# Kernel optimization log

Hardware: AMD Instinct MI355X
Metric: run time of the kernel (lower is better)

Reference implementation:

```python
import jax, jax.numpy as jnp
import numpy as np

TOKENS = 8192
DIM = 4096
N_EXPERTS = 256
TOPK = 8
N_GROUPS = 8
TOPK_GROUPS = 4
ROUTE_SCALE = 2.5


def setup_inputs() -> dict:
    key = jax.random.key(0)
    k1, k2, k3 = jax.random.split(key, 3)
    x = jax.random.normal(k1, (TOKENS, DIM), dtype=jnp.float32)
    W = jax.random.normal(k2, (N_EXPERTS, DIM), dtype=jnp.float32) * (DIM ** -0.5)
    bias = jax.random.normal(k3, (N_EXPERTS,), dtype=jnp.float32) * 0.01
    return {"x": x, "W": W, "bias": bias}


def reference(x, W, bias):
    T = x.shape[0]
    # linear scoring: [T, E]
    logits = jnp.einsum("td,ed->te", x, W)
    scores = jax.nn.sigmoid(logits)  # score_func == 'sigmoid'
    original_scores = scores
    s = scores + bias  # bias-corrected scores used only for routing
    # group-limited routing: [T, G, E/G]
    sg = s.reshape(T, N_GROUPS, -1)
    # bias is not None -> group score = sum of top-2 within each group
    group_scores = jax.lax.top_k(sg, 2)[0].sum(axis=-1)  # [T, G]
    gidx = jax.lax.top_k(group_scores, TOPK_GROUPS)[1]  # [T, topk_groups]
    mask = jnp.zeros((T, N_GROUPS), dtype=s.dtype).at[
        jnp.arange(T)[:, None], gidx
    ].set(1.0)
    s_masked = (sg * mask[:, :, None]).reshape(T, -1)  # [T, E]
    # final top-k over masked scores
    indices = jax.lax.top_k(s_masked, TOPK)[1]  # [T, topk] int32
    weights = jnp.take_along_axis(original_scores, indices, axis=1)
    # sigmoid path: renormalize selected weights
    weights = weights / weights.sum(axis=-1, keepdims=True)
    weights = weights * ROUTE_SCALE
    return weights.astype(x.dtype), indices
```

## Files before the change

kernel.cpp:

```cpp
#include <hip/hip_runtime.h>
#include <math.h>

#define TOKENS 8192
#define DIM 4096
#define NEXP 256
#define TK 8
#define ROUTE_SCALE 2.5f
#define TH1 1e-5f
#define TH2 2e-5f

#define PITCH 40

typedef _Float16 half8 __attribute__((ext_vector_type(8)));
typedef float f4 __attribute__((ext_vector_type(4)));
union H8 { half8 v; int4 q; };

__global__ __launch_bounds__(256) void wsplit(const float* __restrict__ W,
                                              _Float16* __restrict__ Whp,
                                              _Float16* __restrict__ Wlp,
                                              int* __restrict__ flag_cnt) {
    int fi = blockIdx.x * 256 + threadIdx.x;
    if (fi == 0) *flag_cnt = 0;
    int lane = fi & 63;
    int kc = (fi >> 6) & 127;
    int et = fi >> 13;
    int e = et * 16 + (lane & 15);
    int k = kc * 32 + ((lane >> 4) << 3);
    const float* src = W + (size_t)e * DIM + k;
    float4 a = *(const float4*)src;
    float4 b = *(const float4*)(src + 4);
    float f[8] = {a.x, a.y, a.z, a.w, b.x, b.y, b.z, b.w};
    H8 hh, hl;
#pragma unroll
    for (int j = 0; j < 8; j++) {
        float ws = f[j] * 256.0f;
        _Float16 h = (_Float16)ws;
        float r = ws - (float)h;
        hh.v[j] = h;
        hl.v[j] = (_Float16)(r * 2048.0f);
    }
    *(int4*)(Whp + (size_t)fi * 8) = hh.q;
    *(int4*)(Wlp + (size_t)fi * 8) = hl.q;
}

__global__ __launch_bounds__(256, 3) void score_gemm(const float* __restrict__ x,
                                                     const _Float16* __restrict__ Whp,
                                                     const _Float16* __restrict__ Wlp,
                                                     float* __restrict__ parts) {
    __shared__ __align__(16) _Float16 sAh[2][64 * PITCH];
    __shared__ __align__(16) _Float16 sAl[2][64 * PITCH];

    const int m0 = blockIdx.x * 64;
    const int nb = blockIdx.y;
    const int chunk = blockIdx.z;
    const int kcb = 43 * chunk;
    const int kce = kcb + (chunk == 2 ? 42 : 43);

    const int tid = threadIdx.x;
    const int lane = tid & 63;
    const int wave = tid >> 6;
    const int et0 = nb * 8 + wave * 2;

    const int srow = tid >> 2;
    const int scol = (tid & 3) * 8;
    const int sidx = srow * PITCH + scol;
    const float* xrow = x + (size_t)(m0 + srow) * DIM + scol;

    f4 accH[4][2], accC[4][2];
#pragma unroll
    for (int i = 0; i < 4; i++)
#pragma unroll
        for (int j = 0; j < 2; j++) { accH[i][j] = (f4)0.0f; accC[i][j] = (f4)0.0f; }

    float4 ra[2][2];
    half8 bh[2][2], bl[2][2];

#define LOADRAW(S, KC)                                                         \
    {                                                                          \
        const float* p_ = xrow + (size_t)(KC) * 32;                            \
        ra[S][0] = *(const float4*)p_;                                         \
        ra[S][1] = *(const float4*)(p_ + 4);                                   \
    }

#define CONV(S, B_)                                                            \
    {                                                                          \
        float f_[8] = {ra[S][0].x, ra[S][0].y, ra[S][0].z, ra[S][0].w,         \
                       ra[S][1].x, ra[S][1].y, ra[S][1].z, ra[S][1].w};        \
        H8 hh_, hl_;                                                           \
        _Pragma("unroll") for (int j_ = 0; j_ < 8; j_++) {                     \
            float xv_ = f_[j_] * 16.0f;                                        \
            _Float16 hv_ = (_Float16)xv_;                                      \
            float r_ = xv_ - (float)hv_;                                       \
            hh_.v[j_] = hv_;                                                   \
            hl_.v[j_] = (_Float16)(r_ * 2048.0f);                              \
        }                                                                      \
        *(int4*)&sAh[B_][sidx] = hh_.q;                                        \
        *(int4*)&sAl[B_][sidx] = hl_.q;                                        \
    }

#define BLOAD(P_, KC)                                                          \
    _Pragma("unroll") for (int nt_ = 0; nt_ < 2; nt_++) {                      \
        size_t o_ = ((size_t)((et0 + nt_) * 128 + (KC)) * 64 + lane) * 8;      \
        bh[P_][nt_] = *(const half8*)(Whp + o_);                               \
        bl[P_][nt_] = *(const half8*)(Wlp + o_);                               \
    }

#define MFMA_PHASE(P)                                                          \
    _Pragma("unroll") for (int mt_ = 0; mt_ < 4; mt_++) {                      \
        int ra_ = (mt_ * 16 + (lane & 15)) * PITCH + ((lane >> 4) << 3);       \
        half8 ah_ = *(const half8*)&sAh[P][ra_];                               \
        half8 al_ = *(const half8*)&sAl[P][ra_];                               \
        _Pragma("unroll") for (int nt_ = 0; nt_ < 2; nt_++) {                  \
            accH[mt_][nt_] = __builtin_amdgcn_mfma_f32_16x16x32_f16(           \
                ah_, bh[P][nt_], accH[mt_][nt_], 0, 0, 0);                     \
            accC[mt_][nt_] = __builtin_amdgcn_mfma_f32_16x16x32_f16(           \
                ah_, bl[P][nt_], accC[mt_][nt_], 0, 0, 0);                     \
            accC[mt_][nt_] = __builtin_amdgcn_mfma_f32_16x16x32_f16(           \
                al_, bh[P][nt_], accC[mt_][nt_], 0, 0, 0);                     \
        }                                                                      \
    }

#define BARRIER() asm volatile("s_waitcnt lgkmcnt(0)\n\ts_barrier" ::: "memory")

#define ITER(KC, P)                                                            \
    {                                                                          \
        if ((KC) + 1 < kce) { BLOAD(P ^ 1, (KC) + 1) }                         \
        if ((KC) + 2 < kce) { LOADRAW(P, (KC) + 2) }                           \
        MFMA_PHASE(P)                                                          \
        if ((KC) + 1 < kce) { CONV(P ^ 1, P ^ 1) }                             \
        BARRIER();                                                             \
    }

    LOADRAW(0, kcb)
    CONV(0, 0)
    LOADRAW(1, kcb + 1)
    BLOAD(0, kcb)
    BARRIER();

    int kc = kcb;
    while (kc + 2 <= kce) {
        ITER(kc, 0)
        ITER(kc + 1, 1)
        kc += 2;
    }
    if (kc < kce) { ITER(kc, 0) }

    float* pc = parts + (size_t)chunk * TOKENS * NEXP;
#pragma unroll
    for (int mt = 0; mt < 4; mt++)
#pragma unroll
        for (int nt = 0; nt < 2; nt++) {
            int m = m0 + mt * 16 + ((lane >> 4) << 2);
            int e = (et0 + nt) * 16 + (lane & 15);
#pragma unroll
            for (int r = 0; r < 4; r++)
                pc[(size_t)(m + r) * NEXP + e] =
                    accH[mt][nt][r] + accC[mt][nt][r] * (1.0f / 2048.0f);
        }
#undef LOADRAW
#undef CONV
#undef BLOAD
#undef MFMA_PHASE
#undef BARRIER
#undef ITER
}

__global__ __launch_bounds__(256) void route_kernel(const float* __restrict__ parts,
                                                    const float* __restrict__ bias,
                                                    float* __restrict__ out_w,
                                                    float* __restrict__ out_i,
                                                    int* __restrict__ flag_cnt,
                                                    int* __restrict__ flag_list) {
    const int t = blockIdx.x * 4 + (threadIdx.x >> 6);
    const int l = threadIdx.x & 63;

    const float* p = parts + (size_t)t * NEXP + (l << 2);
    float4 q0 = *(const float4*)p;
    float4 q1 = *(const float4*)(p + (size_t)TOKENS * NEXP);
    float4 q2 = *(const float4*)(p + (size_t)2 * TOKENS * NEXP);
    float4 b4 = *(const float4*)&bias[l << 2];
    float sc[4], sb[4];
    {
        float lg0 = (q0.x + q1.x + q2.x) * (1.0f / 4096.0f);
        float lg1 = (q0.y + q1.y + q2.y) * (1.0f / 4096.0f);
        float lg2 = (q0.z + q1.z + q2.z) * (1.0f / 4096.0f);
        float lg3 = (q0.w + q1.w + q2.w) * (1.0f / 4096.0f);
        sc[0] = 1.0f / (1.0f + expf(-lg0));
        sc[1] = 1.0f / (1.0f + expf(-lg1));
        sc[2] = 1.0f / (1.0f + expf(-lg2));
        sc[3] = 1.0f / (1.0f + expf(-lg3));
        sb[0] = sc[0] + b4.x; sb[1] = sc[1] + b4.y;
        sb[2] = sc[2] + b4.z; sb[3] = sc[3] + b4.w;
    }

    float v1 = sb[0], v2 = -1e30f, v3 = -1e30f;
#pragma unroll
    for (int c = 1; c < 4; c++) {
        float xv = sb[c];
        if (xv > v1) { v3 = v2; v2 = v1; v1 = xv; }
        else if (xv > v2) { v3 = v2; v2 = xv; }
        else if (xv > v3) { v3 = xv; }
    }

#pragma unroll
    for (int m = 1; m < 8; m <<= 1) {
        float o1 = __shfl_xor(v1, m, 64);
        float o2 = __shfl_xor(v2, m, 64);
        float o3 = __shfl_xor(v3, m, 64);
        bool aw = (v1 >= o1);
        float A1 = aw ? v1 : o1, A2 = aw ? v2 : o2, A3 = aw ? v3 : o3;
        float B1 = aw ? o1 : v1, B2 = aw ? o2 : v2;
        float n2, n3;
        if (A2 >= B1) { n2 = A2; n3 = fmaxf(B1, A3); }
        else          { n2 = B1; n3 = fmaxf(A2, B2); }
        v1 = A1; v2 = n2; v3 = n3;
    }
    float gscore = v1 + v2;
    float gap23 = v2 - v3;
#pragma unroll
    for (int m = 8; m < 64; m <<= 1) gap23 = fminf(gap23, __shfl_xor(gap23, m, 64));

    float gs[8];
#pragma unroll
    for (int g = 0; g < 8; g++) gs[g] = __shfl(gscore, g << 3, 64);

    const int mygrp = l >> 3;
    int rank = 0;
#pragma unroll
    for (int g = 0; g < 8; g++) {
        bool better = (gs[g] > gscore) || (gs[g] == gscore && g < mygrp);
        rank += (g != mygrp && better) ? 1 : 0;
    }
    const bool sel = rank < 4;

    float minsel = 1e30f, maxuns = -1e30f;
#pragma unroll
    for (int g = 0; g < 8; g++) {
        int rg = 0;
#pragma unroll
        for (int g2 = 0; g2 < 8; g2++)
            rg += (g2 != g && ((gs[g2] > gs[g]) || (gs[g2] == gs[g] && g2 < g))) ? 1 : 0;
        if (rg < 4) minsel = fminf(minsel, gs[g]); else maxuns = fmaxf(maxuns, gs[g]);
    }
    float gap45 = minsel - maxuns;

    float cand[4];
#pragma unroll
    for (int c = 0; c < 4; c++) cand[c] = sel ? sb[c] : 0.0f;

    float wv[8], wi[8], vb[9];
    float wsum = 0.0f;
#pragma unroll
    for (int r = 0; r < 9; r++) {
        float v = cand[0];
        int idx = (l << 2);
#pragma unroll
        for (int c = 1; c < 4; c++) {
            if (cand[c] > v) { v = cand[c]; idx = (l << 2) + c; }
        }
#pragma unroll
        for (int m = 32; m >= 1; m >>= 1) {
            float ov = __shfl_xor(v, m, 64);
            int oi = __shfl_xor(idx, m, 64);
            if (ov > v || (ov == v && oi < idx)) { v = ov; idx = oi; }
        }
        vb[r] = v;
        if (r < 8) {
            const int cc = idx & 3;
            const bool own = (idx >> 2) == l;
            cand[0] = (own && cc == 0) ? -__builtin_inff() : cand[0];
            cand[1] = (own && cc == 1) ? -__builtin_inff() : cand[1];
            cand[2] = (own && cc == 2) ? -__builtin_inff() : cand[2];
            cand[3] = (own && cc == 3) ? -__builtin_inff() : cand[3];
            float tmp = (cc == 0) ? sc[0] : (cc == 1) ? sc[1] : (cc == 2) ? sc[2] : sc[3];
            float ws = __shfl(tmp, idx >> 2, 64);
            wv[r] = ws;
            wi[r] = (float)idx;
            wsum += ws;
        }
    }
    float mingap = 1e30f;
#pragma unroll
    for (int r = 0; r < 8; r++) mingap = fminf(mingap, vb[r] - vb[r + 1]);

    const float scale = ROUTE_SCALE / wsum;
    if (l == 0) {
        float* ow = out_w + (size_t)t * TK;
        float* oi = out_i + (size_t)t * TK;
#pragma unroll
        for (int r = 0; r < 8; r++) ow[r] = wv[r] * scale;
#pragma unroll
        for (int r = 0; r < 8; r++) oi[r] = wi[r];
        if (gap23 < TH1 || gap45 < TH2 || mingap < TH1) {
            int pos = atomicAdd(flag_cnt, 1);
            flag_list[pos] = t;
        }
    }
}

__global__ __launch_bounds__(256) void fixup_kernel(const float* __restrict__ x,
                                                    const float* __restrict__ W,
                                                    const float* __restrict__ bias,
                                                    const int* __restrict__ flag_cnt,
                                                    const int* __restrict__ flag_list,
                                                    float* __restrict__ out_w,
                                                    float* __restrict__ out_i) {
    __shared__ float S[NEXP];
    const int n = *flag_cnt;
    for (int i = blockIdx.x; i < n; i += gridDim.x) {
        const int t = flag_list[i];
        const float* xr = x + (size_t)t * DIM;
        const float* wr = W + (size_t)threadIdx.x * DIM;
        float acc = 0.0f;
        for (int k = 0; k < DIM; k += 4) {
            float4 xv = *(const float4*)(xr + k);
            float4 wv = *(const float4*)(wr + k);
            acc = fmaf(xv.x, wv.x, acc);
            acc = fmaf(xv.y, wv.y, acc);
            acc = fmaf(xv.z, wv.z, acc);
            acc = fmaf(xv.w, wv.w, acc);
        }
        S[threadIdx.x] = 1.0f / (1.0f + expf(-acc));
        __syncthreads();
        if (threadIdx.x < 64) {
            const int l = threadIdx.x;
            float sc[4] = {S[4 * l], S[4 * l + 1], S[4 * l + 2], S[4 * l + 3]};
            float4 b4 = *(const float4*)&bias[4 * l];
            float sb[4] = {sc[0] + b4.x, sc[1] + b4.y, sc[2] + b4.z, sc[3] + b4.w};

            float h1 = fmaxf(sb[0], sb[1]), q1 = fminf(sb[0], sb[1]);
            float h2 = fmaxf(sb[2], sb[3]), q2 = fminf(sb[2], sb[3]);
            float m1 = fmaxf(h1, h2);
            float m2 = fmaxf(fminf(h1, h2), fmaxf(q1, q2));
#pragma unroll
            for (int m = 1; m < 8; m <<= 1) {
                float o1 = __shfl_xor(m1, m, 64);
                float o2 = __shfl_xor(m2, m, 64);
                float nm1 = fmaxf(m1, o1);
                float nm2 = fmaxf(fminf(m1, o1), fmaxf(m2, o2));
                m1 = nm1; m2 = nm2;
            }
            float gscore = m1 + m2;
            float gs[8];
#pragma unroll
            for (int g = 0; g < 8; g++) gs[g] = __shfl(gscore, g << 3, 64);
            const int mygrp = l >> 3;
            int rank = 0;
#pragma unroll
            for (int g = 0; g < 8; g++) {
                bool better = (gs[g] > gscore) || (gs[g] == gscore && g < mygrp);
                rank += (g != mygrp && better) ? 1 : 0;
            }
            const bool selg = rank < 4;
            float cand[4];
#pragma unroll
            for (int c = 0; c < 4; c++) cand[c] = selg ? sb[c] : 0.0f;
            float wv[8], wi[8];
            float wsum = 0.0f;
#pragma unroll
            for (int r = 0; r < 8; r++) {
                float v = cand[0];
                int idx = (l << 2);
#pragma unroll
                for (int c = 1; c < 4; c++) {
                    if (cand[c] > v) { v = cand[c]; idx = (l << 2) + c; }
                }
#pragma unroll
                for (int m = 32; m >= 1; m >>= 1) {
                    float ov = __shfl_xor(v, m, 64);
                    int oi = __shfl_xor(idx, m, 64);
                    if (ov > v || (ov == v && oi < idx)) { v = ov; idx = oi; }
                }
                const int cc = idx & 3;
                const bool own = (idx >> 2) == l;
                cand[0] = (own && cc == 0) ? -__builtin_inff() : cand[0];
                cand[1] = (own && cc == 1) ? -__builtin_inff() : cand[1];
                cand[2] = (own && cc == 2) ? -__builtin_inff() : cand[2];
                cand[3] = (own && cc == 3) ? -__builtin_inff() : cand[3];
                float tmp = (cc == 0) ? sc[0] : (cc == 1) ? sc[1] : (cc == 2) ? sc[2] : sc[3];
                float ws = __shfl(tmp, idx >> 2, 64);
                wv[r] = ws;
                wi[r] = (float)idx;
                wsum += ws;
            }
            const float scale = ROUTE_SCALE / wsum;
            if (l == 0) {
                float* ow = out_w + (size_t)t * TK;
                float* oi = out_i + (size_t)t * TK;
#pragma unroll
                for (int r = 0; r < 8; r++) ow[r] = wv[r] * scale;
#pragma unroll
                for (int r = 0; r < 8; r++) oi[r] = wi[r];
            }
        }
        __syncthreads();
    }
}

extern "C" void kernel_launch(void* const* d_in, const int* in_sizes, int n_in,
                              void* d_out, int out_size, void* d_ws, size_t ws_size,
                              hipStream_t stream) {
    const float* x = (const float*)d_in[0];
    const float* W = (const float*)d_in[1];
    const float* bias = (const float*)d_in[2];
    float* out = (float*)d_out;

    char* ws = (char*)d_ws;
    float* parts = (float*)ws;
    _Float16* Whp = (_Float16*)(ws + (size_t)3 * TOKENS * NEXP * 4);
    _Float16* Wlp = Whp + (size_t)NEXP * DIM;
    int* flag_cnt = (int*)((char*)(Wlp + (size_t)NEXP * DIM));
    int* flag_list = flag_cnt + 4;

    wsplit<<<512, 256, 0, stream>>>(W, Whp, Wlp, flag_cnt);

    dim3 gGemm(TOKENS / 64, 2, 3);
    score_gemm<<<gGemm, 256, 0, stream>>>(x, Whp, Wlp, parts);

    route_kernel<<<TOKENS / 4, 256, 0, stream>>>(parts, bias, out,
                                                 out + (size_t)TOKENS * TK,
                                                 flag_cnt, flag_list);
    fixup_kernel<<<1024, 256, 0, stream>>>(x, W, bias, flag_cnt, flag_list,
                                           out, out + (size_t)TOKENS * TK);
}
```

Measured before the change: 363.4 us.

## Stage x in LDS and software-pipeline W row loads in fixup kernel

The fixup kernel now copies each flagged token's x row into shared memory and keeps a large register buffer of W values, prefetching the next chunk while computing the current one. The grid shrinks from 1024 to 256 blocks with launch bounds allowing one block per CU. This targets the latency of serially streaming a 16KB W row per thread. The cost is very high register use, with a risk of spills, and less parallelism across flagged tokens.

```diff
diff --git a/kernel.cpp b/kernel.cpp
--- a/kernel.cpp
+++ b/kernel.cpp
@@ -298,27 +298,54 @@
     }
 }
 
-__global__ __launch_bounds__(256) void fixup_kernel(const float* __restrict__ x,
-                                                    const float* __restrict__ W,
-                                                    const float* __restrict__ bias,
-                                                    const int* __restrict__ flag_cnt,
-                                                    const int* __restrict__ flag_list,
-                                                    float* __restrict__ out_w,
-                                                    float* __restrict__ out_i) {
+__global__ __launch_bounds__(256, 1) void fixup_kernel(const float* __restrict__ x,
+                                                       const float* __restrict__ W,
+                                                       const float* __restrict__ bias,
+                                                       const int* __restrict__ flag_cnt,
+                                                       const int* __restrict__ flag_list,
+                                                       float* __restrict__ out_w,
+                                                       float* __restrict__ out_i) {
     __shared__ float S[NEXP];
+    __shared__ __align__(16) float sx[DIM];
     const int n = *flag_cnt;
     for (int i = blockIdx.x; i < n; i += gridDim.x) {
         const int t = flag_list[i];
         const float* xr = x + (size_t)t * DIM;
+#pragma unroll
+        for (int j = 0; j < 4; j++) {
+            const int idx = (j * 256 + threadIdx.x) * 4;
+            *(float4*)&sx[idx] = *(const float4*)(xr + idx);
+        }
+        __syncthreads();
+
         const float* wr = W + (size_t)threadIdx.x * DIM;
+        float4 wb[8][8];
+#pragma unroll
+        for (int d = 0; d < 8; d++)
+#pragma unroll
+            for (int q = 0; q < 8; q++)
+                wb[d][q] = *(const float4*)(wr + d * 32 + q * 4);
+
         float acc = 0.0f;
-        for (int k = 0; k < DIM; k += 4) {
-            float4 xv = *(const float4*)(xr + k);
-            float4 wv = *(const float4*)(wr + k);
-            acc = fmaf(xv.x, wv.x, acc);
-            acc = fmaf(xv.y, wv.y, acc);
-            acc = fmaf(xv.z, wv.z, acc);
-            acc = fmaf(xv.w, wv.w, acc);
+        for (int s16 = 0; s16 < 16; s16++) {
+#pragma unroll
+            for (int d = 0; d < 8; d++) {
+                const int s = s16 * 8 + d;
+#pragma unroll
+                for (int q = 0; q < 8; q++) {
+                    const float4 wv = wb[d][q];
+                    const float4 xv = *(const float4*)&sx[s * 32 + q * 4];
+                    acc = fmaf(xv.x, wv.x, acc);
+                    acc = fmaf(xv.y, wv.y, acc);
+                    acc = fmaf(xv.z, wv.z, acc);
+                    acc = fmaf(xv.w, wv.w, acc);
+                }
+                if (s16 < 15) {
+#pragma unroll
+                    for (int q = 0; q < 8; q++)
+                        wb[d][q] = *(const float4*)(wr + (s + 8) * 32 + q * 4);
+                }
+            }
         }
         S[threadIdx.x] = 1.0f / (1.0f + expf(-acc));
         __syncthreads();
@@ -420,6 +447,6 @@
     route_kernel<<<TOKENS / 4, 256, 0, stream>>>(parts, bias, out,
                                                  out + (size_t)TOKENS * TK,
                                                  flag_cnt, flag_list);
-    fixup_kernel<<<1024, 256, 0, stream>>>(x, W, bias, flag_cnt, flag_list,
-                                           out, out + (size_t)TOKENS * TK);
+    fixup_kernel<<<256, 256, 0, stream>>>(x, W, bias, flag_cnt, flag_list,
+                                          out, out + (size_t)TOKENS * TK);
 }
```

Result: slower. 371.9 us (+2.3%).

## Pipeline fixup kernel W loads through LDS with async global-to-LDS ring buffer

Applied to the files above, without the earlier changes.

Rewrites the exact fp32 fixup kernel so that the token row is staged once in shared memory and W columns stream through a 4-deep LDS ring using global_load_lds with XOR swizzling. The old version had each thread read its own strided W row and the x row straight from global memory. The new version aims to coalesce loads and overlap the memory traffic with the FMAs. It also cuts the grid from 1024 to 256 blocks with launch_bounds(256,1), which trades occupancy for explicit pipelining and risks lower throughput when many tokens are flagged.

```diff
diff --git a/kernel.cpp b/kernel.cpp
--- a/kernel.cpp
+++ b/kernel.cpp
@@ -298,32 +298,87 @@
     }
 }
 
-__global__ __launch_bounds__(256) void fixup_kernel(const float* __restrict__ x,
-                                                    const float* __restrict__ W,
-                                                    const float* __restrict__ bias,
-                                                    const int* __restrict__ flag_cnt,
-                                                    const int* __restrict__ flag_list,
-                                                    float* __restrict__ out_w,
-                                                    float* __restrict__ out_i) {
+__device__ __forceinline__ void gload16(const float* g, float* l) {
+    __builtin_amdgcn_global_load_lds(
+        (const __attribute__((address_space(1))) void*)g,
+        (__attribute__((address_space(3))) void*)l, 16, 0, 0);
+}
+
+__global__ __launch_bounds__(256, 1) void fixup_kernel(const float* __restrict__ x,
+                                                       const float* __restrict__ W,
+                                                       const float* __restrict__ bias,
+                                                       const int* __restrict__ flag_cnt,
+                                                       const int* __restrict__ flag_list,
+                                                       float* __restrict__ out_w,
+                                                       float* __restrict__ out_i) {
     __shared__ float S[NEXP];
+    __shared__ __align__(16) float sx[DIM];
+    __shared__ __align__(16) float ring[4][NEXP * 32];
+
+    const int tid = threadIdx.x;
+    const int lane = tid & 63;
+    const int wave = tid >> 6;
+
+#define STAGE(P, C)                                                            \
+    {                                                                          \
+        const int e_ = wave * 64 + (lane >> 3);                                \
+        const int q_ = (lane & 7) ^ ((lane >> 3) & 7);                         \
+        _Pragma("unroll") for (int j_ = 0; j_ < 8; j_++) {                     \
+            gload16(W + (size_t)(e_ + j_ * 8) * DIM + (C) * 32 + q_ * 4,       \
+                    &ring[P][(wave * 8 + j_) * 256]);                          \
+        }                                                                      \
+    }
+
+#define COMPUTE(P, C)                                                          \
+    {                                                                          \
+        const float* xb_ = sx + (C) * 32;                                      \
+        _Pragma("unroll") for (int q_ = 0; q_ < 8; q_++) {                     \
+            const int qq_ = q_ ^ (tid & 7);                                    \
+            const float4 wv = *(const float4*)&ring[P][tid * 32 + qq_ * 4];    \
+            const float4 xv = *(const float4*)(xb_ + q_ * 4);                  \
+            acc = fmaf(xv.x, wv.x, acc);                                       \
+            acc = fmaf(xv.y, wv.y, acc);                                       \
+            acc = fmaf(xv.z, wv.z, acc);                                       \
+            acc = fmaf(xv.w, wv.w, acc);                                       \
+        }                                                                      \
+    }
+
+#define PBAR() asm volatile("s_barrier" ::: "memory")
+#define WAITV(N) asm volatile("s_waitcnt vmcnt(" #N ")" ::: "memory")
+
     const int n = *flag_cnt;
     for (int i = blockIdx.x; i < n; i += gridDim.x) {
         const int t = flag_list[i];
         const float* xr = x + (size_t)t * DIM;
-        const float* wr = W + (size_t)threadIdx.x * DIM;
+#pragma unroll
+        for (int j = 0; j < 4; j++) {
+            const int idx = (j * 256 + tid) * 4;
+            *(float4*)&sx[idx] = *(const float4*)(xr + idx);
+        }
+        __syncthreads();
+
+        STAGE(0, 0)
+        STAGE(1, 1)
+        STAGE(2, 2)
+
         float acc = 0.0f;
-        for (int k = 0; k < DIM; k += 4) {
-            float4 xv = *(const float4*)(xr + k);
-            float4 wv = *(const float4*)(wr + k);
-            acc = fmaf(xv.x, wv.x, acc);
-            acc = fmaf(xv.y, wv.y, acc);
-            acc = fmaf(xv.z, wv.z, acc);
-            acc = fmaf(xv.w, wv.w, acc);
-        }
-        S[threadIdx.x] = 1.0f / (1.0f + expf(-acc));
+        for (int c = 0; c < 126; c++) {
+            WAITV(16);
+            PBAR();
+            if (c + 3 < 128) { STAGE((c + 3) & 3, c + 3) }
+            COMPUTE(c & 3, c)
+        }
+        WAITV(8);
+        PBAR();
+        COMPUTE(2, 126)
+        WAITV(0);
+        PBAR();
+        COMPUTE(3, 127)
+
+        S[tid] = 1.0f / (1.0f + expf(-acc));
         __syncthreads();
-        if (threadIdx.x < 64) {
-            const int l = threadIdx.x;
+        if (tid < 64) {
+            const int l = tid;
             float sc[4] = {S[4 * l], S[4 * l + 1], S[4 * l + 2], S[4 * l + 3]};
             float4 b4 = *(const float4*)&bias[4 * l];
             float sb[4] = {sc[0] + b4.x, sc[1] + b4.y, sc[2] + b4.z, sc[3] + b4.w};
@@ -395,6 +450,10 @@
         }
         __syncthreads();
     }
+#undef STAGE
+#undef COMPUTE
+#undef PBAR
+#undef WAITV
 }
 
 extern "C" void kernel_launch(void* const* d_in, const int* in_sizes, int n_in,
@@ -420,6 +479,6 @@
     route_kernel<<<TOKENS / 4, 256, 0, stream>>>(parts, bias, out,
                                                  out + (size_t)TOKENS * TK,
                                                  flag_cnt, flag_list);
-    fixup_kernel<<<1024, 256, 0, stream>>>(x, W, bias, flag_cnt, flag_list,
-                                           out, out + (size_t)TOKENS * TK);
-}
+    fixup_kernel<<<256, 256, 0, stream>>>(x, W, bias, flag_cnt, flag_list,
+                                          out, out + (size_t)TOKENS * TK);
+}
```

Result: faster. 355.7 us (-2.1%).

## Stage x row in LDS and software-pipeline W loads in fixup kernel

Applied to the files above, without the earlier changes.

The fixup kernel now copies the flagged token's x row into shared memory once per token and reads W through a four-stage register ring buffer, issuing loads for later chunks while earlier chunks are consumed. This aims to hide global-load latency in the FP32 recomputation of flagged tokens. The grid shrinks from 1024 to 256 blocks and launch bounds request one block per SM, which raises register pressure from the 128-float buffer and lowers parallelism when many tokens are flagged.

```diff
diff --git a/kernel.cpp b/kernel.cpp
--- a/kernel.cpp
+++ b/kernel.cpp
@@ -298,32 +298,73 @@
     }
 }
 
-__global__ __launch_bounds__(256) void fixup_kernel(const float* __restrict__ x,
-                                                    const float* __restrict__ W,
-                                                    const float* __restrict__ bias,
-                                                    const int* __restrict__ flag_cnt,
-                                                    const int* __restrict__ flag_list,
-                                                    float* __restrict__ out_w,
-                                                    float* __restrict__ out_i) {
+__global__ __launch_bounds__(256, 1) void fixup_kernel(const float* __restrict__ x,
+                                                       const float* __restrict__ W,
+                                                       const float* __restrict__ bias,
+                                                       const int* __restrict__ flag_cnt,
+                                                       const int* __restrict__ flag_list,
+                                                       float* __restrict__ out_w,
+                                                       float* __restrict__ out_i) {
     __shared__ float S[NEXP];
+    __shared__ __align__(16) float sx[DIM];
+    const int tid = threadIdx.x;
+
+#define FILL(BUF, S_)                                                          \
+    _Pragma("unroll") for (int q_ = 0; q_ < 8; q_++)                           \
+        BUF[q_] = *(const float4*)(wr + (S_) * 32 + q_ * 4);
+
+#define CONSUME(BUF, S_)                                                       \
+    {                                                                          \
+        const float* xb_ = sx + (S_) * 32;                                     \
+        _Pragma("unroll") for (int q_ = 0; q_ < 8; q_++) {                     \
+            const float4 wv = BUF[q_];                                         \
+            const float4 xv = *(const float4*)(xb_ + q_ * 4);                  \
+            acc = fmaf(xv.x, wv.x, acc);                                       \
+            acc = fmaf(xv.y, wv.y, acc);                                       \
+            acc = fmaf(xv.z, wv.z, acc);                                       \
+            acc = fmaf(xv.w, wv.w, acc);                                       \
+        }                                                                      \
+    }
+
     const int n = *flag_cnt;
     for (int i = blockIdx.x; i < n; i += gridDim.x) {
         const int t = flag_list[i];
         const float* xr = x + (size_t)t * DIM;
-        const float* wr = W + (size_t)threadIdx.x * DIM;
+#pragma unroll
+        for (int j = 0; j < 4; j++) {
+            const int idx = (j * 256 + tid) * 4;
+            *(float4*)&sx[idx] = *(const float4*)(xr + idx);
+        }
+        __syncthreads();
+
+        const float* wr = W + (size_t)tid * DIM;
+        float4 wb0[8], wb1[8], wb2[8], wb3[8];
+        FILL(wb0, 0)
+        FILL(wb1, 1)
+        FILL(wb2, 2)
+        FILL(wb3, 3)
+
         float acc = 0.0f;
-        for (int k = 0; k < DIM; k += 4) {
-            float4 xv = *(const float4*)(xr + k);
-            float4 wv = *(const float4*)(wr + k);
-            acc = fmaf(xv.x, wv.x, acc);
-            acc = fmaf(xv.y, wv.y, acc);
-            acc = fmaf(xv.z, wv.z, acc);
-            acc = fmaf(xv.w, wv.w, acc);
-        }
-        S[threadIdx.x] = 1.0f / (1.0f + expf(-acc));
+        for (int c4 = 0; c4 < 31; c4++) {
+            const int s = c4 * 4;
+            CONSUME(wb0, s)
+            FILL(wb0, s + 4)
+            CONSUME(wb1, s + 1)
+            FILL(wb1, s + 5)
+            CONSUME(wb2, s + 2)
+            FILL(wb2, s + 6)
+            CONSUME(wb3, s + 3)
+            FILL(wb3, s + 7)
+        }
+        CONSUME(wb0, 124)
+        CONSUME(wb1, 125)
+        CONSUME(wb2, 126)
+        CONSUME(wb3, 127)
+
+        S[tid] = 1.0f / (1.0f + expf(-acc));
         __syncthreads();
-        if (threadIdx.x < 64) {
-            const int l = threadIdx.x;
+        if (tid < 64) {
+            const int l = tid;
             float sc[4] = {S[4 * l], S[4 * l + 1], S[4 * l + 2], S[4 * l + 3]};
             float4 b4 = *(const float4*)&bias[4 * l];
             float sb[4] = {sc[0] + b4.x, sc[1] + b4.y, sc[2] + b4.z, sc[3] + b4.w};
@@ -395,6 +436,8 @@
         }
         __syncthreads();
     }
+#undef FILL
+#undef CONSUME
 }
 
 extern "C" void kernel_launch(void* const* d_in, const int* in_sizes, int n_in,
@@ -420,6 +463,6 @@
     route_kernel<<<TOKENS / 4, 256, 0, stream>>>(parts, bias, out,
                                                  out + (size_t)TOKENS * TK,
                                                  flag_cnt, flag_list);
-    fixup_kernel<<<1024, 256, 0, stream>>>(x, W, bias, flag_cnt, flag_list,
-                                           out, out + (size_t)TOKENS * TK);
+    fixup_kernel<<<256, 256, 0, stream>>>(x, W, bias, flag_cnt, flag_list,
+                                          out, out + (size_t)TOKENS * TK);
 }
```

Result: no change. 365.0 us (+0.4%).
